# Kernel optimization log

Hardware: AMD Instinct MI355X
Metric: run time of the kernel (lower is better)

## Reference

```python
import jax, jax.numpy as jnp
import numpy as np

B, S, D, H, DK, DL, DR = 2, 2048, 2048, 16, 128, 512, 64
EPS = 1e-6


def _rmsnorm(x, w):
    # torch nn.RMSNorm: x / sqrt(mean(x^2) + eps) * weight, over last dim
    return x * jax.lax.rsqrt(jnp.mean(x * x, axis=-1, keepdims=True) + EPS) * w


def _rope_tables(seq_len, d):
    # matches RoPE.__init__: half of the d//2 freqs are real, half are zero
    quarter = d // 4
    freq = (1.0 / 10000.0) ** jnp.linspace(0.0, 1.0, quarter, dtype=jnp.float32)
    freq = jnp.concatenate([freq, jnp.zeros((quarter,), jnp.float32)])
    theta = jnp.arange(seq_len, dtype=jnp.float32)[:, None] * freq[None, :]  # (S, d//2)
    return jnp.cos(theta), jnp.sin(theta)


def _apply_rope(x, cos, sin):
    # x: (B, H, S, d); cos/sin: (S, d//2)
    half = x.shape[-1] // 2
    x1, x2 = x[..., :half], x[..., half:]
    c = cos[None, None, :, :]
    s = sin[None, None, :, :]
    y1 = x1 * c + x2 * s
    y2 = -x1 * s + x2 * c
    return jnp.concatenate([y1, y2], axis=-1)


def setup_inputs() -> dict:
    key = jax.random.key(0)
    ks = jax.random.split(key, 9)
    w = lambda k, sh: jax.random.normal(k, sh, jnp.float32) * 0.02
    return {
        "x": jax.random.normal(ks[0], (B, S, D), jnp.float32),
        "wq": w(ks[1], (D, H * DK)),
        "w_kv_down": w(ks[2], (D, DL)),
        "w_k_rope": w(ks[3], (DL, H * DR)),
        "w_k_nope": w(ks[4], (DL, H * (DK - DR))),
        "wv": w(ks[5], (DL, H * DK)),
        "wo": w(ks[6], (H * DK, D)),
        "q_norm_w": jnp.ones((DK,), jnp.float32),
        "k_norm_w": jnp.ones((DK,), jnp.float32),
    }


def reference(x, wq, w_kv_down, w_k_rope, w_k_nope, wv, wo, q_norm_w, k_norm_w):
    b, s, _ = x.shape
    # Q path
    q = (x @ wq).reshape(b, s, H, DK)
    q = _rmsnorm(q, q_norm_w).transpose(0, 2, 1, 3)  # (B,H,S,DK)
    # low-rank KV latent
    latent = x @ w_kv_down  # (B,S,DL)
    v = (latent @ wv).reshape(b, s, H, DK).transpose(0, 2, 1, 3)
    k_rope = (latent @ w_k_rope).reshape(b, s, H, DR).transpose(0, 2, 1, 3)
    k_nope = (latent @ w_k_nope).reshape(b, s, H, DK - DR).transpose(0, 2, 1, 3)
    # decoupled RoPE on first DR dims of q and on k_rope
    cos, sin = _rope_tables(s, DR)
    q = jnp.concatenate([_apply_rope(q[..., :DR], cos, sin), q[..., DR:]], axis=-1)
    k = jnp.concatenate([_apply_rope(k_rope, cos, sin), k_nope], axis=-1)
    k = _rmsnorm(k, k_norm_w)
    # causal SDPA, scale 1/sqrt(DK)
    scale = 1.0 / np.sqrt(DK).astype(np.float32)
    scores = jnp.einsum('bhqd,bhkd->bhqk', q, k) * scale
    causal = jnp.tril(jnp.ones((s, s), bool))
    scores = jnp.where(causal[None, None], scores, jnp.finfo(scores.dtype).min)
    attn = jax.nn.softmax(scores, axis=-1)
    out = jnp.einsum('bhqk,bhkd->bhqd', attn, v)
    out = out.transpose(0, 2, 1, 3).reshape(b, s, H * DK)
    return out @ wo
```

## Files before the change

kernel.cpp:

```cpp
#include <hip/hip_runtime.h>
#include <hip/hip_bf16.h>
#include <math.h>

#define B_ 2
#define S_ 2048
#define D_ 2048
#define H_ 16
#define DK_ 128
#define DL_ 512
#define DR_ 64
#define BS_ (B_ * S_)

typedef __attribute__((ext_vector_type(8))) short short8;
typedef __attribute__((ext_vector_type(4))) float f32x4;

static __device__ __forceinline__ ushort f2b(float f) {
    union { __hip_bfloat16 h; ushort u; } cvt;
    cvt.h = __float2bfloat16(f);
    return cvt.u;
}

#define GLOAD_LDS16(g, l)                                                         \
    __builtin_amdgcn_global_load_lds(                                             \
        (const __attribute__((address_space(1))) void*)(g),                       \
        (__attribute__((address_space(3))) void*)(l), 16, 0, 0)

__global__ __launch_bounds__(256) void cvt_f32_bf16(const float* __restrict__ in,
                                                    ushort* __restrict__ out, int n) {
    int i = (blockIdx.x * 256 + threadIdx.x) * 4;
    if (i >= n) return;
    float4 v = *(const float4*)(in + i);
    ushort4 o;
    o.x = f2b(v.x); o.y = f2b(v.y); o.z = f2b(v.z); o.w = f2b(v.w);
    *(ushort4*)(out + i) = o;
}

__global__ __launch_bounds__(256) void transpose_cvt(const float* __restrict__ in,
                                                     ushort* __restrict__ out,
                                                     int R, int C) {
    __shared__ float tile[32][33];
    int c0 = blockIdx.x * 32, r0 = blockIdx.y * 32;
    int tx = threadIdx.x, ty = threadIdx.y;
#pragma unroll
    for (int i = 0; i < 4; ++i)
        tile[ty + i * 8][tx] = in[(size_t)(r0 + ty + i * 8) * C + c0 + tx];
    __syncthreads();
#pragma unroll
    for (int i = 0; i < 4; ++i)
        out[(size_t)(c0 + ty + i * 8) * R + r0 + tx] = f2b(tile[tx][ty + i * 8]);
}

__global__ __launch_bounds__(256) void v_transpose(const ushort* __restrict__ vb,
                                                   ushort* __restrict__ vt) {
    __shared__ ushort tile[32][34];
    const int bh = blockIdx.z, b = bh >> 4, h = bh & 15;
    const int d0 = blockIdx.x * 32, s0 = blockIdx.y * 32;
    const int tx = threadIdx.x, ty = threadIdx.y;
    const ushort* src = vb + (size_t)(b * 2048 + s0) * 2048 + h * 128 + d0;
#pragma unroll
    for (int i = 0; i < 4; ++i)
        tile[ty + i * 8][tx] = src[(size_t)(ty + i * 8) * 2048 + tx];
    __syncthreads();
    ushort* dst = vt + ((size_t)bh * 128 + d0) * 2048 + s0;
#pragma unroll
    for (int i = 0; i < 4; ++i)
        dst[(size_t)(ty + i * 8) * 2048 + tx] = tile[tx][ty + i * 8];
}

__global__ __launch_bounds__(256) void rope_tables(float* __restrict__ cosT,
                                                   float* __restrict__ sinT) {
    int idx = blockIdx.x * 256 + threadIdx.x;
    int s = idx >> 5, j = idx & 31;
    float c = 1.f, sn = 0.f;
    if (j < 16) {
        float t = (float)j * (1.0f / 15.0f);
        float f = powf(10000.0f, -t);
        float th = (float)s * f;
        c = cosf(th);
        sn = sinf(th);
    }
    cosT[idx] = c;
    sinT[idx] = sn;
}

template <int OUT_BF16>
__global__ __launch_bounds__(256) void gemm_bt(const ushort* __restrict__ A,
                                               const ushort* __restrict__ BT,
                                               void* __restrict__ Cv,
                                               int M, int N, int K) {
    __shared__ __align__(16) ushort As[128 * 32];
    __shared__ __align__(16) ushort Bs[128 * 32];
    const int tid = threadIdx.x;
    const int lane = tid & 63, wave = tid >> 6;
    const int wr = wave >> 1, wc = wave & 1;
    const int row0 = blockIdx.y * 128, col0 = blockIdx.x * 128;
    const int fr = lane & 15, kg = (lane >> 4) * 8;

    f32x4 acc[4][4] = {};

    const int sr = tid >> 2;
    const int sc8 = (tid & 3) * 8;
    const ushort* ga = A + (size_t)(row0 + sr) * K + sc8;
    const ushort* gb = BT + (size_t)(col0 + sr) * K + sc8;
    ushort* asDst = As + (size_t)(wave * 64) * 8;
    ushort* bsDst = Bs + (size_t)(wave * 64) * 8;

    for (int k0 = 0; k0 < K; k0 += 32) {
        GLOAD_LDS16(ga + k0, asDst);
        GLOAD_LDS16(ga + (size_t)64 * K + k0, asDst + 256 * 8);
        GLOAD_LDS16(gb + k0, bsDst);
        GLOAD_LDS16(gb + (size_t)64 * K + k0, bsDst + 256 * 8);
        __syncthreads();

        short8 af[4], bfr[4];
#pragma unroll
        for (int m = 0; m < 4; ++m)
            af[m] = *(const short8*)&As[(wr * 64 + m * 16 + fr) * 32 + kg];
#pragma unroll
        for (int n = 0; n < 4; ++n)
            bfr[n] = *(const short8*)&Bs[(wc * 64 + n * 16 + fr) * 32 + kg];
#pragma unroll
        for (int m = 0; m < 4; ++m)
#pragma unroll
            for (int n = 0; n < 4; ++n)
                acc[m][n] = __builtin_amdgcn_mfma_f32_16x16x32_bf16(af[m], bfr[n],
                                                                    acc[m][n], 0, 0, 0);
        __syncthreads();
    }

    const int rbase = row0 + wr * 64 + (lane >> 4) * 4;
    const int cbase = col0 + wc * 64 + fr;
    if constexpr (OUT_BF16) {
        ushort* C = (ushort*)Cv;
#pragma unroll
        for (int m = 0; m < 4; ++m)
#pragma unroll
            for (int n = 0; n < 4; ++n)
#pragma unroll
                for (int j = 0; j < 4; ++j)
                    C[(size_t)(rbase + m * 16 + j) * N + cbase + n * 16] = f2b(acc[m][n][j]);
    } else {
        float* C = (float*)Cv;
#pragma unroll
        for (int m = 0; m < 4; ++m)
#pragma unroll
            for (int n = 0; n < 4; ++n)
#pragma unroll
                for (int j = 0; j < 4; ++j)
                    C[(size_t)(rbase + m * 16 + j) * N + cbase + n * 16] = acc[m][n][j];
    }
}

__global__ __launch_bounds__(256) void q_norm_rope(const float* __restrict__ qp,
                                                   const float* __restrict__ w,
                                                   const float* __restrict__ cosT,
                                                   const float* __restrict__ sinT,
                                                   ushort* __restrict__ qb) {
    const int lane = threadIdx.x & 63, wave = threadIdx.x >> 6;
    const int rowId = blockIdx.x * 4 + wave;
    const int bs = rowId >> 4, h = rowId & 15;
    const int s = bs & (S_ - 1);
    const float scale = 0.08838834764831845f;
    const float* src = qp + (size_t)bs * 2048 + h * 128;
    float e0 = src[lane], e1 = src[64 + lane];
    float ss = e0 * e0 + e1 * e1;
#pragma unroll
    for (int m = 1; m < 64; m <<= 1) ss += __shfl_xor(ss, m, 64);
    float r = rsqrtf(ss * (1.0f / 128.0f) + 1e-6f);
    float xn0 = e0 * r * w[lane];
    float xn1 = e1 * r * w[64 + lane];
    int j = lane & 31;
    float c = cosT[s * 32 + j], sn = sinT[s * 32 + j];
    float p = __shfl_xor(xn0, 32, 64);
    float y0 = (lane < 32) ? (xn0 * c + p * sn) : (-p * sn + xn0 * c);
    ushort* dst = qb + (size_t)bs * 2048 + h * 128;
    dst[lane] = f2b(y0 * scale);
    dst[64 + lane] = f2b(xn1 * scale);
}

__global__ __launch_bounds__(256) void k_assemble(const float* __restrict__ krp,
                                                  const float* __restrict__ knp,
                                                  const float* __restrict__ w,
                                                  const float* __restrict__ cosT,
                                                  const float* __restrict__ sinT,
                                                  ushort* __restrict__ kb) {
    const int lane = threadIdx.x & 63, wave = threadIdx.x >> 6;
    const int rowId = blockIdx.x * 4 + wave;
    const int bs = rowId >> 4, h = rowId & 15;
    const int s = bs & (S_ - 1);
    float e0 = krp[(size_t)bs * 1024 + h * 64 + lane];
    float e1 = knp[(size_t)bs * 1024 + h * 64 + lane];
    int j = lane & 31;
    float c = cosT[s * 32 + j], sn = sinT[s * 32 + j];
    float p = __shfl_xor(e0, 32, 64);
    float y0 = (lane < 32) ? (e0 * c + p * sn) : (-p * sn + e0 * c);
    float ss = y0 * y0 + e1 * e1;
#pragma unroll
    for (int m = 1; m < 64; m <<= 1) ss += __shfl_xor(ss, m, 64);
    float r = rsqrtf(ss * (1.0f / 128.0f) + 1e-6f);
    ushort* dst = kb + (size_t)bs * 2048 + h * 128;
    dst[lane] = f2b(y0 * r * w[lane]);
    dst[64 + lane] = f2b(e1 * r * w[64 + lane]);
}

__global__ __launch_bounds__(512) void attn_fwd(const ushort* __restrict__ Q,
                                                const ushort* __restrict__ Kb,
                                                const ushort* __restrict__ Vt,
                                                ushort* __restrict__ Ob) {
    __shared__ __align__(16) ushort Kls[2][8192];
    __shared__ __align__(16) ushort Vls[2][8192];
    __shared__ __align__(16) ushort Pls[8][1024];
    const int tid = threadIdx.x, lane = tid & 63, wave = tid >> 6;
    const int bh = blockIdx.y, b = bh >> 4, h = bh & 15;
    const int fr = lane & 15, g = lane >> 4;
    const int sfr = lane >> 2, sg = lane & 3;

    const ushort* qbase = Q + (size_t)(b * S_) * 2048 + h * 128;
    const ushort* kbase = Kb + (size_t)(b * S_) * 2048 + h * 128;
    const ushort* vtbase = Vt + (size_t)bh * 128 * 2048;
    ushort* myP = Pls[wave];

    auto stage = [&](int kt0, int bufi) {
#pragma unroll
        for (int i = 0; i < 2; ++i) {
            const int si = wave * 2 + i;
            GLOAD_LDS16(kbase + (size_t)(kt0 + (si >> 2) * 16 + sfr) * 2048 +
                            (si & 3) * 32 + sg * 8,
                        &Kls[bufi][si * 512]);
            GLOAD_LDS16(vtbase + (size_t)((si >> 1) * 16 + sfr) * 2048 + kt0 +
                            (si & 1) * 32 + sg * 8,
                        &Vls[bufi][si * 512]);
        }
    };

#pragma unroll 1
    for (int pi = 0; pi < 2; ++pi) {
        const int qi = pi ? (int)blockIdx.x : 15 - (int)blockIdx.x;
        const int q0 = qi * 128;
        const int nt = 2 * qi + 2;

        short8 qf[4];
        const ushort* qrow = qbase + (size_t)(q0 + wave * 16 + fr) * 2048;
#pragma unroll
        for (int kb = 0; kb < 4; ++kb) qf[kb] = *(const short8*)(qrow + kb * 32 + g * 8);

        f32x4 Oacc[8] = {};
        float mrow[4], lrow[4];
#pragma unroll
        for (int j = 0; j < 4; ++j) { mrow[j] = -1e30f; lrow[j] = 0.f; }

        stage(0, 0);
        for (int t = 0; t < nt; ++t) {
            __syncthreads();
            if (t + 1 < nt) stage((t + 1) * 64, (t + 1) & 1);
            const ushort* Kc = Kls[t & 1];
            const ushort* Vc = Vls[t & 1];
            const int kt0 = t * 64;
            f32x4 sc[4] = {};
#pragma unroll
            for (int n = 0; n < 4; ++n)
#pragma unroll
                for (int kb = 0; kb < 4; ++kb) {
                    short8 kf = *(const short8*)&Kc[(n * 4 + kb) * 512 + fr * 32 + g * 8];
                    sc[n] = __builtin_amdgcn_mfma_f32_16x16x32_bf16(qf[kb], kf, sc[n], 0, 0, 0);
                }
            if (t >= nt - 2) {
#pragma unroll
                for (int n = 0; n < 4; ++n) {
                    int kpos = kt0 + n * 16 + fr;
#pragma unroll
                    for (int j = 0; j < 4; ++j) {
                        int qr = q0 + wave * 16 + g * 4 + j;
                        if (kpos > qr) sc[n][j] = -1e30f;
                    }
                }
            }
            float tmax[4];
#pragma unroll
            for (int j = 0; j < 4; ++j)
                tmax[j] = fmaxf(fmaxf(sc[0][j], sc[1][j]), fmaxf(sc[2][j], sc[3][j]));
#pragma unroll
            for (int m = 1; m < 16; m <<= 1)
#pragma unroll
                for (int j = 0; j < 4; ++j) tmax[j] = fmaxf(tmax[j], __shfl_xor(tmax[j], m, 64));
            float alpha[4], rsum[4];
#pragma unroll
            for (int j = 0; j < 4; ++j) {
                float mn = fmaxf(mrow[j], tmax[j]);
                alpha[j] = __expf(mrow[j] - mn);
                mrow[j] = mn;
                rsum[j] = 0.f;
            }
#pragma unroll
            for (int n = 0; n < 4; ++n)
#pragma unroll
                for (int j = 0; j < 4; ++j) {
                    float pv = __expf(sc[n][j] - mrow[j]);
                    sc[n][j] = pv;
                    rsum[j] += pv;
                }
#pragma unroll
            for (int m = 1; m < 16; m <<= 1)
#pragma unroll
                for (int j = 0; j < 4; ++j) rsum[j] += __shfl_xor(rsum[j], m, 64);
#pragma unroll
            for (int j = 0; j < 4; ++j) lrow[j] = lrow[j] * alpha[j] + rsum[j];
#pragma unroll
            for (int n8 = 0; n8 < 8; ++n8)
#pragma unroll
                for (int j = 0; j < 4; ++j) Oacc[n8][j] *= alpha[j];
#pragma unroll
            for (int n = 0; n < 4; ++n)
#pragma unroll
                for (int j = 0; j < 4; ++j) {
                    int q = g * 4 + j;
                    int cg = n * 2 + (fr >> 3);
                    int cs = (((cg ^ q) & 7) << 3) | (fr & 7);
                    myP[q * 64 + cs] = f2b(sc[n][j]);
                }
            short8 pa[2];
#pragma unroll
            for (int ks = 0; ks < 2; ++ks) {
                int pg = ((ks * 4 + g) ^ fr) & 7;
                pa[ks] = *(const short8*)&myP[fr * 64 + (pg << 3)];
            }
#pragma unroll
            for (int n8 = 0; n8 < 8; ++n8)
#pragma unroll
                for (int ks = 0; ks < 2; ++ks) {
                    short8 vf = *(const short8*)&Vc[(n8 * 2 + ks) * 512 + fr * 32 + g * 8];
                    Oacc[n8] = __builtin_amdgcn_mfma_f32_16x16x32_bf16(pa[ks], vf, Oacc[n8], 0, 0, 0);
                }
        }
#pragma unroll
        for (int j = 0; j < 4; ++j) {
            int qr = q0 + wave * 16 + g * 4 + j;
            float inv = 1.0f / lrow[j];
            ushort* orow = Ob + (size_t)(b * S_ + qr) * 2048 + h * 128;
#pragma unroll
            for (int n8 = 0; n8 < 8; ++n8) orow[n8 * 16 + fr] = f2b(Oacc[n8][j] * inv);
        }
        __syncthreads();
    }
}

extern "C" void kernel_launch(void* const* d_in, const int* in_sizes, int n_in,
                              void* d_out, int out_size, void* d_ws, size_t ws_size,
                              hipStream_t stream) {
    (void)in_sizes; (void)n_in; (void)out_size; (void)ws_size;
    const float* x = (const float*)d_in[0];
    const float* wq = (const float*)d_in[1];
    const float* w_kv_down = (const float*)d_in[2];
    const float* w_k_rope = (const float*)d_in[3];
    const float* w_k_nope = (const float*)d_in[4];
    const float* wv = (const float*)d_in[5];
    const float* wo = (const float*)d_in[6];
    const float* q_norm_w = (const float*)d_in[7];
    const float* k_norm_w = (const float*)d_in[8];
    float* out = (float*)d_out;

    char* ws = (char*)d_ws;
    size_t off = 0;
    auto alloc = [&](size_t bytes) {
        off = (off + 255) & ~(size_t)255;
        void* p = ws + off;
        off += bytes;
        return p;
    };
    ushort* xb = (ushort*)alloc((size_t)BS_ * 2048 * 2);
    ushort* wq_t = (ushort*)alloc((size_t)2048 * 2048 * 2);
    ushort* wkv_t = (ushort*)alloc((size_t)512 * 2048 * 2);
    ushort* wkr_t = (ushort*)alloc((size_t)1024 * 512 * 2);
    ushort* wkn_t = (ushort*)alloc((size_t)1024 * 512 * 2);
    ushort* wv_t = (ushort*)alloc((size_t)2048 * 512 * 2);
    ushort* wo_t = (ushort*)alloc((size_t)2048 * 2048 * 2);
    float* q_pre = (float*)alloc((size_t)BS_ * 2048 * 4);
    ushort* latent_b = (ushort*)alloc((size_t)BS_ * 512 * 2);
    float* kr_pre = (float*)alloc((size_t)BS_ * 1024 * 4);
    float* kn_pre = (float*)alloc((size_t)BS_ * 1024 * 4);
    ushort* v_b = (ushort*)alloc((size_t)BS_ * 2048 * 2);
    ushort* q_b = (ushort*)alloc((size_t)BS_ * 2048 * 2);
    ushort* k_b = (ushort*)alloc((size_t)BS_ * 2048 * 2);
    ushort* ao_b = (ushort*)alloc((size_t)BS_ * 2048 * 2);
    float* cosT = (float*)alloc((size_t)S_ * 32 * 4);
    float* sinT = (float*)alloc((size_t)S_ * 32 * 4);
    ushort* vt = (ushort*)q_pre;

    cvt_f32_bf16<<<(BS_ * 2048 / 4 + 255) / 256, 256, 0, stream>>>(x, xb, BS_ * 2048);
    transpose_cvt<<<dim3(2048 / 32, 2048 / 32), dim3(32, 8), 0, stream>>>(wq, wq_t, 2048, 2048);
    transpose_cvt<<<dim3(512 / 32, 2048 / 32), dim3(32, 8), 0, stream>>>(w_kv_down, wkv_t, 2048, 512);
    transpose_cvt<<<dim3(1024 / 32, 512 / 32), dim3(32, 8), 0, stream>>>(w_k_rope, wkr_t, 512, 1024);
    transpose_cvt<<<dim3(1024 / 32, 512 / 32), dim3(32, 8), 0, stream>>>(w_k_nope, wkn_t, 512, 1024);
    transpose_cvt<<<dim3(2048 / 32, 512 / 32), dim3(32, 8), 0, stream>>>(wv, wv_t, 512, 2048);
    transpose_cvt<<<dim3(2048 / 32, 2048 / 32), dim3(32, 8), 0, stream>>>(wo, wo_t, 2048, 2048);
    rope_tables<<<S_ * 32 / 256, 256, 0, stream>>>(cosT, sinT);

    gemm_bt<0><<<dim3(2048 / 128, BS_ / 128), 256, 0, stream>>>(xb, wq_t, q_pre, BS_, 2048, 2048);
    gemm_bt<1><<<dim3(512 / 128, BS_ / 128), 256, 0, stream>>>(xb, wkv_t, latent_b, BS_, 512, 2048);
    gemm_bt<0><<<dim3(1024 / 128, BS_ / 128), 256, 0, stream>>>(latent_b, wkr_t, kr_pre, BS_, 1024, 512);
    gemm_bt<0><<<dim3(1024 / 128, BS_ / 128), 256, 0, stream>>>(latent_b, wkn_t, kn_pre, BS_, 1024, 512);
    gemm_bt<1><<<dim3(2048 / 128, BS_ / 128), 256, 0, stream>>>(latent_b, wv_t, v_b, BS_, 2048, 512);

    q_norm_rope<<<BS_ * H_ / 4, 256, 0, stream>>>(q_pre, q_norm_w, cosT, sinT, q_b);
    k_assemble<<<BS_ * H_ / 4, 256, 0, stream>>>(kr_pre, kn_pre, k_norm_w, cosT, sinT, k_b);

    v_transpose<<<dim3(128 / 32, 2048 / 32, B_ * H_), dim3(32, 8), 0, stream>>>(v_b, vt);

    attn_fwd<<<dim3(8, B_ * H_), 512, 0, stream>>>(q_b, k_b, vt, ao_b);

    gemm_bt<0><<<dim3(2048 / 128, BS_ / 128), 256, 0, stream>>>(ao_b, wo_t, out, BS_, 2048, 2048);
}
```

Before: 480.1 us.

## Fuse latent up-projections, store bf16 intermediates, lazy softmax rescale, tweak attention scheduling

Concatenates the k_rope, k_nope and V up-projection weights so one GEMM produces all three as bf16, and stores the Q projection as bf16 instead of fp32. This cuts launches and intermediate memory traffic. The attention kernel gains several changes: a remapped block index so blocks of the same query-pair index are spread across heads, s_setprio around the MFMA sections, and a different LDS swizzle for P. It also skips the online-softmax rescale when the running max grows by no more than 8, which risks fp32 exp overflow or precision loss in the accumulators. Rounding Q and K to bf16 before the norm adds some error.

```diff
diff --git a/kernel.cpp b/kernel.cpp
--- a/kernel.cpp
+++ b/kernel.cpp
@@ -19,6 +19,9 @@
     cvt.h = __float2bfloat16(f);
     return cvt.u;
 }
+static __device__ __forceinline__ float b2f(ushort u) {
+    return __uint_as_float(((uint)u) << 16);
+}
 
 #define GLOAD_LDS16(g, l)                                                         \
     __builtin_amdgcn_global_load_lds(                                             \
@@ -50,16 +53,16 @@
         out[(size_t)(c0 + ty + i * 8) * R + r0 + tx] = f2b(tile[tx][ty + i * 8]);
 }
 
-__global__ __launch_bounds__(256) void v_transpose(const ushort* __restrict__ vb,
+__global__ __launch_bounds__(256) void v_transpose(const ushort* __restrict__ krnv,
                                                    ushort* __restrict__ vt) {
     __shared__ ushort tile[32][34];
     const int bh = blockIdx.z, b = bh >> 4, h = bh & 15;
     const int d0 = blockIdx.x * 32, s0 = blockIdx.y * 32;
     const int tx = threadIdx.x, ty = threadIdx.y;
-    const ushort* src = vb + (size_t)(b * 2048 + s0) * 2048 + h * 128 + d0;
+    const ushort* src = krnv + (size_t)(b * 2048 + s0) * 4096 + 2048 + h * 128 + d0;
 #pragma unroll
     for (int i = 0; i < 4; ++i)
-        tile[ty + i * 8][tx] = src[(size_t)(ty + i * 8) * 2048 + tx];
+        tile[ty + i * 8][tx] = src[(size_t)(ty + i * 8) * 4096 + tx];
     __syncthreads();
     ushort* dst = vt + ((size_t)bh * 128 + d0) * 2048 + s0;
 #pragma unroll
@@ -151,7 +154,7 @@
     }
 }
 
-__global__ __launch_bounds__(256) void q_norm_rope(const float* __restrict__ qp,
+__global__ __launch_bounds__(256) void q_norm_rope(const ushort* __restrict__ qp,
                                                    const float* __restrict__ w,
                                                    const float* __restrict__ cosT,
                                                    const float* __restrict__ sinT,
@@ -161,8 +164,8 @@
     const int bs = rowId >> 4, h = rowId & 15;
     const int s = bs & (S_ - 1);
     const float scale = 0.08838834764831845f;
-    const float* src = qp + (size_t)bs * 2048 + h * 128;
-    float e0 = src[lane], e1 = src[64 + lane];
+    const ushort* src = qp + (size_t)bs * 2048 + h * 128;
+    float e0 = b2f(src[lane]), e1 = b2f(src[64 + lane]);
     float ss = e0 * e0 + e1 * e1;
 #pragma unroll
     for (int m = 1; m < 64; m <<= 1) ss += __shfl_xor(ss, m, 64);
@@ -178,8 +181,7 @@
     dst[64 + lane] = f2b(xn1 * scale);
 }
 
-__global__ __launch_bounds__(256) void k_assemble(const float* __restrict__ krp,
-                                                  const float* __restrict__ knp,
+__global__ __launch_bounds__(256) void k_assemble(const ushort* __restrict__ krnv,
                                                   const float* __restrict__ w,
                                                   const float* __restrict__ cosT,
                                                   const float* __restrict__ sinT,
@@ -188,8 +190,8 @@
     const int rowId = blockIdx.x * 4 + wave;
     const int bs = rowId >> 4, h = rowId & 15;
     const int s = bs & (S_ - 1);
-    float e0 = krp[(size_t)bs * 1024 + h * 64 + lane];
-    float e1 = knp[(size_t)bs * 1024 + h * 64 + lane];
+    float e0 = b2f(krnv[(size_t)bs * 4096 + h * 64 + lane]);
+    float e1 = b2f(krnv[(size_t)bs * 4096 + 1024 + h * 64 + lane]);
     int j = lane & 31;
     float c = cosT[s * 32 + j], sn = sinT[s * 32 + j];
     float p = __shfl_xor(e0, 32, 64);
@@ -211,7 +213,9 @@
     __shared__ __align__(16) ushort Vls[2][8192];
     __shared__ __align__(16) ushort Pls[8][1024];
     const int tid = threadIdx.x, lane = tid & 63, wave = tid >> 6;
-    const int bh = blockIdx.y, b = bh >> 4, h = bh & 15;
+    const int bh = (int)blockIdx.x * 4 + ((int)blockIdx.y & 3);
+    const int qp = (int)blockIdx.y >> 2;
+    const int b = bh >> 4, h = bh & 15;
     const int fr = lane & 15, g = lane >> 4;
     const int sfr = lane >> 2, sg = lane & 3;
 
@@ -235,7 +239,7 @@
 
 #pragma unroll 1
     for (int pi = 0; pi < 2; ++pi) {
-        const int qi = pi ? (int)blockIdx.x : 15 - (int)blockIdx.x;
+        const int qi = pi ? qp : 15 - qp;
         const int q0 = qi * 128;
         const int nt = 2 * qi + 2;
 
@@ -257,6 +261,7 @@
             const ushort* Vc = Vls[t & 1];
             const int kt0 = t * 64;
             f32x4 sc[4] = {};
+            __builtin_amdgcn_s_setprio(1);
 #pragma unroll
             for (int n = 0; n < 4; ++n)
 #pragma unroll
@@ -264,6 +269,7 @@
                     short8 kf = *(const short8*)&Kc[(n * 4 + kb) * 512 + fr * 32 + g * 8];
                     sc[n] = __builtin_amdgcn_mfma_f32_16x16x32_bf16(qf[kb], kf, sc[n], 0, 0, 0);
                 }
+            __builtin_amdgcn_s_setprio(0);
             if (t >= nt - 2) {
 #pragma unroll
                 for (int n = 0; n < 4; ++n) {
@@ -283,14 +289,23 @@
             for (int m = 1; m < 16; m <<= 1)
 #pragma unroll
                 for (int j = 0; j < 4; ++j) tmax[j] = fmaxf(tmax[j], __shfl_xor(tmax[j], m, 64));
-            float alpha[4], rsum[4];
-#pragma unroll
-            for (int j = 0; j < 4; ++j) {
-                float mn = fmaxf(mrow[j], tmax[j]);
-                alpha[j] = __expf(mrow[j] - mn);
-                mrow[j] = mn;
-                rsum[j] = 0.f;
+            float dm = fmaxf(fmaxf(tmax[0] - mrow[0], tmax[1] - mrow[1]),
+                             fmaxf(tmax[2] - mrow[2], tmax[3] - mrow[3]));
+            if (!__all(dm <= 8.0f)) {
+                float alpha[4];
+#pragma unroll
+                for (int j = 0; j < 4; ++j) {
+                    float mn = fmaxf(mrow[j], tmax[j]);
+                    alpha[j] = __expf(mrow[j] - mn);
+                    mrow[j] = mn;
+                    lrow[j] *= alpha[j];
+                }
+#pragma unroll
+                for (int n8 = 0; n8 < 8; ++n8)
+#pragma unroll
+                    for (int j = 0; j < 4; ++j) Oacc[n8][j] *= alpha[j];
             }
+            float rsum[4] = {0.f, 0.f, 0.f, 0.f};
 #pragma unroll
             for (int n = 0; n < 4; ++n)
 #pragma unroll
@@ -304,26 +319,23 @@
 #pragma unroll
                 for (int j = 0; j < 4; ++j) rsum[j] += __shfl_xor(rsum[j], m, 64);
 #pragma unroll
-            for (int j = 0; j < 4; ++j) lrow[j] = lrow[j] * alpha[j] + rsum[j];
-#pragma unroll
-            for (int n8 = 0; n8 < 8; ++n8)
-#pragma unroll
-                for (int j = 0; j < 4; ++j) Oacc[n8][j] *= alpha[j];
+            for (int j = 0; j < 4; ++j) lrow[j] += rsum[j];
 #pragma unroll
             for (int n = 0; n < 4; ++n)
 #pragma unroll
                 for (int j = 0; j < 4; ++j) {
                     int q = g * 4 + j;
                     int cg = n * 2 + (fr >> 3);
-                    int cs = (((cg ^ q) & 7) << 3) | (fr & 7);
+                    int cs = (((cg ^ (q >> 1)) & 7) << 3) | (fr & 7);
                     myP[q * 64 + cs] = f2b(sc[n][j]);
                 }
             short8 pa[2];
 #pragma unroll
             for (int ks = 0; ks < 2; ++ks) {
-                int pg = ((ks * 4 + g) ^ fr) & 7;
+                int pg = ((ks * 4 + g) ^ (fr >> 1)) & 7;
                 pa[ks] = *(const short8*)&myP[fr * 64 + (pg << 3)];
             }
+            __builtin_amdgcn_s_setprio(1);
 #pragma unroll
             for (int n8 = 0; n8 < 8; ++n8)
 #pragma unroll
@@ -331,6 +343,7 @@
                     short8 vf = *(const short8*)&Vc[(n8 * 2 + ks) * 512 + fr * 32 + g * 8];
                     Oacc[n8] = __builtin_amdgcn_mfma_f32_16x16x32_bf16(pa[ks], vf, Oacc[n8], 0, 0, 0);
                 }
+            __builtin_amdgcn_s_setprio(0);
         }
 #pragma unroll
         for (int j = 0; j < 4; ++j) {
@@ -370,41 +383,35 @@
     ushort* xb = (ushort*)alloc((size_t)BS_ * 2048 * 2);
     ushort* wq_t = (ushort*)alloc((size_t)2048 * 2048 * 2);
     ushort* wkv_t = (ushort*)alloc((size_t)512 * 2048 * 2);
-    ushort* wkr_t = (ushort*)alloc((size_t)1024 * 512 * 2);
-    ushort* wkn_t = (ushort*)alloc((size_t)1024 * 512 * 2);
-    ushort* wv_t = (ushort*)alloc((size_t)2048 * 512 * 2);
+    ushort* wkrnv_t = (ushort*)alloc((size_t)4096 * 512 * 2);
     ushort* wo_t = (ushort*)alloc((size_t)2048 * 2048 * 2);
-    float* q_pre = (float*)alloc((size_t)BS_ * 2048 * 4);
+    ushort* q_pre_b = (ushort*)alloc((size_t)BS_ * 2048 * 2);
     ushort* latent_b = (ushort*)alloc((size_t)BS_ * 512 * 2);
-    float* kr_pre = (float*)alloc((size_t)BS_ * 1024 * 4);
-    float* kn_pre = (float*)alloc((size_t)BS_ * 1024 * 4);
-    ushort* v_b = (ushort*)alloc((size_t)BS_ * 2048 * 2);
+    ushort* krnv_b = (ushort*)alloc((size_t)BS_ * 4096 * 2);
     ushort* q_b = (ushort*)alloc((size_t)BS_ * 2048 * 2);
     ushort* k_b = (ushort*)alloc((size_t)BS_ * 2048 * 2);
+    ushort* vt = (ushort*)alloc((size_t)BS_ * 2048 * 2);
     ushort* ao_b = (ushort*)alloc((size_t)BS_ * 2048 * 2);
     float* cosT = (float*)alloc((size_t)S_ * 32 * 4);
     float* sinT = (float*)alloc((size_t)S_ * 32 * 4);
-    ushort* vt = (ushort*)q_pre;
 
     cvt_f32_bf16<<<(BS_ * 2048 / 4 + 255) / 256, 256, 0, stream>>>(x, xb, BS_ * 2048);
     transpose_cvt<<<dim3(2048 / 32, 2048 / 32), dim3(32, 8), 0, stream>>>(wq, wq_t, 2048, 2048);
     transpose_cvt<<<dim3(512 / 32, 2048 / 32), dim3(32, 8), 0, stream>>>(w_kv_down, wkv_t, 2048, 512);
-    transpose_cvt<<<dim3(1024 / 32, 512 / 32), dim3(32, 8), 0, stream>>>(w_k_rope, wkr_t, 512, 1024);
-    transpose_cvt<<<dim3(1024 / 32, 512 / 32), dim3(32, 8), 0, stream>>>(w_k_nope, wkn_t, 512, 1024);
-    transpose_cvt<<<dim3(2048 / 32, 512 / 32), dim3(32, 8), 0, stream>>>(wv, wv_t, 512, 2048);
+    transpose_cvt<<<dim3(1024 / 32, 512 / 32), dim3(32, 8), 0, stream>>>(w_k_rope, wkrnv_t, 512, 1024);
+    transpose_cvt<<<dim3(1024 / 32, 512 / 32), dim3(32, 8), 0, stream>>>(w_k_nope, wkrnv_t + (size_t)1024 * 512, 512, 1024);
+    transpose_cvt<<<dim3(2048 / 32, 512 / 32), dim3(32, 8), 0, stream>>>(wv, wkrnv_t + (size_t)2048 * 512, 512, 2048);
     transpose_cvt<<<dim3(2048 / 32, 2048 / 32), dim3(32, 8), 0, stream>>>(wo, wo_t, 2048, 2048);
     rope_tables<<<S_ * 32 / 256, 256, 0, stream>>>(cosT, sinT);
 
-    gemm_bt<0><<<dim3(2048 / 128, BS_ / 128), 256, 0, stream>>>(xb, wq_t, q_pre, BS_, 2048, 2048);
+    gemm_bt<1><<<dim3(2048 / 128, BS_ / 128), 256, 0, stream>>>(xb, wq_t, q_pre_b, BS_, 2048, 2048);
     gemm_bt<1><<<dim3(512 / 128, BS_ / 128), 256, 0, stream>>>(xb, wkv_t, latent_b, BS_, 512, 2048);
-    gemm_bt<0><<<dim3(1024 / 128, BS_ / 128), 256, 0, stream>>>(latent_b, wkr_t, kr_pre, BS_, 1024, 512);
-    gemm_bt<0><<<dim3(1024 / 128, BS_ / 128), 256, 0, stream>>>(latent_b, wkn_t, kn_pre, BS_, 1024, 512);
-    gemm_bt<1><<<dim3(2048 / 128, BS_ / 128), 256, 0, stream>>>(latent_b, wv_t, v_b, BS_, 2048, 512);
-
-    q_norm_rope<<<BS_ * H_ / 4, 256, 0, stream>>>(q_pre, q_norm_w, cosT, sinT, q_b);
-    k_assemble<<<BS_ * H_ / 4, 256, 0, stream>>>(kr_pre, kn_pre, k_norm_w, cosT, sinT, k_b);
-
-    v_transpose<<<dim3(128 / 32, 2048 / 32, B_ * H_), dim3(32, 8), 0, stream>>>(v_b, vt);
+    gemm_bt<1><<<dim3(4096 / 128, BS_ / 128), 256, 0, stream>>>(latent_b, wkrnv_t, krnv_b, BS_, 4096, 512);
+
+    q_norm_rope<<<BS_ * H_ / 4, 256, 0, stream>>>(q_pre_b, q_norm_w, cosT, sinT, q_b);
+    k_assemble<<<BS_ * H_ / 4, 256, 0, stream>>>(krnv_b, k_norm_w, cosT, sinT, k_b);
+
+    v_transpose<<<dim3(128 / 32, 2048 / 32, B_ * H_), dim3(32, 8), 0, stream>>>(krnv_b, vt);
 
     attn_fwd<<<dim3(8, B_ * H_), 512, 0, stream>>>(q_b, k_b, vt, ao_b);
 
```

Result: faster. 455.3 us (-5.2%).
